# Kernel tuning notes

Hardware: AMD Instinct MI355X
Metric: run time of the kernel (lower is better)

The kernel has to match this reference:

```python
import jax, jax.numpy as jnp
import numpy as np
from jax import lax

EPS = 0.01  # BatchNorm eps from the module

def binarize(x):
    # BinarizeF: >= 0 -> +1, < 0 -> -1
    return jnp.where(x >= 0, 1.0, -1.0).astype(x.dtype)

def bintanh(x):
    # binarize(hardtanh(x)); clip doesn't change sign so forward == sign
    return binarize(jnp.clip(x, -1.0, 1.0))

def bn_nch(x, g, b, m, v):
    # BatchNorm1d eval mode over channel axis of [B, C, L]
    scale = g / jnp.sqrt(v + EPS)
    return (x - m[None, :, None]) * scale[None, :, None] + b[None, :, None]

def bn_nc(x, g, b, m, v):
    scale = g / jnp.sqrt(v + EPS)
    return (x - m[None, :]) * scale[None, :] + b[None, :]

def setup_inputs() -> dict:
    key = jax.random.key(0)
    ks = jax.random.split(key, 32)
    B, CIN, W = 65536, 4, 16
    C, H = 32, 64
    d = {
        'x': jax.random.normal(ks[0], (B, CIN, W), jnp.float32),
        'conv0_w': jax.random.normal(ks[1], (C, CIN, 1), jnp.float32) * 0.1,
        'conv0_b': jax.random.normal(ks[2], (C,), jnp.float32) * 0.01,
        'bn0_g': jax.random.uniform(ks[3], (C,), jnp.float32, 0.5, 1.5),
        'bn0_b': jax.random.normal(ks[4], (C,), jnp.float32) * 0.1,
        'bn0_m': jax.random.normal(ks[5], (C,), jnp.float32) * 0.1,
        'bn0_v': jnp.ones((C,), jnp.float32),
        'convs_w': jax.random.normal(ks[6], (4, C, C, 3), jnp.float32) * 0.1,
        'convs_b': jax.random.normal(ks[7], (4, C), jnp.float32) * 0.01,
        'bns_g': jax.random.uniform(ks[8], (4, C), jnp.float32, 0.5, 1.5),
        'bns_b': jax.random.normal(ks[9], (4, C), jnp.float32) * 0.1,
        'bns_m': jax.random.normal(ks[10], (4, C), jnp.float32) * 0.1,
        'bns_v': jnp.ones((4, C), jnp.float32),
        'fc1_w': jax.random.normal(ks[11], (H, C * W), jnp.float32) * 0.05,
        'fc1_b': jax.random.normal(ks[12], (H,), jnp.float32) * 0.01,
        'bn5_g': jax.random.uniform(ks[13], (H,), jnp.float32, 0.5, 1.5),
        'bn5_b': jax.random.normal(ks[14], (H,), jnp.float32) * 0.1,
        'bn5_m': jax.random.normal(ks[15], (H,), jnp.float32) * 0.1,
        'bn5_v': jnp.ones((H,), jnp.float32),
        'fc2_w': jax.random.normal(ks[16], (H, H), jnp.float32) * 0.1,
        'fc2_b': jax.random.normal(ks[17], (H,), jnp.float32) * 0.01,
        'bn6_g': jax.random.uniform(ks[18], (H,), jnp.float32, 0.5, 1.5),
        'bn6_b': jax.random.normal(ks[19], (H,), jnp.float32) * 0.1,
        'bn6_m': jax.random.normal(ks[20], (H,), jnp.float32) * 0.1,
        'bn6_v': jnp.ones((H,), jnp.float32),
        'fc3_w': jax.random.normal(ks[21], (1, H), jnp.float32) * 0.1,
        'fc3_b': jax.random.normal(ks[22], (1,), jnp.float32) * 0.01,
    }
    return d

def reference(x, conv0_w, conv0_b, bn0_g, bn0_b, bn0_m, bn0_v,
              convs_w, convs_b, bns_g, bns_b, bns_m, bns_v,
              fc1_w, fc1_b, bn5_g, bn5_b, bn5_m, bn5_v,
              fc2_w, fc2_b, bn6_g, bn6_b, bn6_m, bn6_v,
              fc3_w, fc3_b):
    B = x.shape[0]
    x = x.reshape(-1, 4, 16)  # (B, n_inputs, word_size)
    # conv0: kernel_size=1 binarized conv -> pointwise channel mix
    y = jnp.einsum('bci,oc->boi', x, binarize(conv0_w[:, :, 0])) + conv0_b[None, :, None]
    y = bintanh(bn_nch(y, bn0_g, bn0_b, bn0_m, bn0_v))
    shortcut = y
    dn = ('NCH', 'OIH', 'NCH')
    for i in range(convs_w.shape[0]):  # numLayers - 1 = 4 fixed blocks
        z = lax.conv_general_dilated(y, binarize(convs_w[i]), (1,), ((1, 1),),
                                     dimension_numbers=dn)
        z = z + convs_b[i][None, :, None]
        z = bn_nch(z, bns_g[i], bns_b[i], bns_m[i], bns_v[i])
        y = bintanh(z) + shortcut  # residual add to first block output
    f = y.reshape(B, -1)  # (B, 32*16)
    h = bintanh(bn_nc(f @ binarize(fc1_w).T + fc1_b, bn5_g, bn5_b, bn5_m, bn5_v))
    h = bintanh(bn_nc(h @ binarize(fc2_w).T + fc2_b, bn6_g, bn6_b, bn6_m, bn6_v))
    out = jax.nn.sigmoid(h @ binarize(fc3_w).T + fc3_b)  # (B, 1)
    return out
```

## Files before the change

### kernel.cpp

```cpp
#include <hip/hip_runtime.h>
#include <hip/hip_bf16.h>
#include <math.h>

typedef unsigned int uint;

#define WB4   0
#define L1S   512
#define L1T   640
#define W1T   672
#define T5O   1696
#define W2T   1760
#define T6O   1888
#define W3O   1952
#define FB3O  1954
#define TOTW  1955

#define ST5   (T5O - W1T)
#define SW2   (W2T - W1T)
#define ST6   (T6O - W1T)
#define SW3   (W3O - W1T)
#define SFB3  (FB3O - W1T)
#define SMTOT (TOTW - W1T)

__device__ __forceinline__ float bnr(float v, float cb, float m, float sc, float b) {
  return __fadd_rn(__fmul_rn(__fsub_rn(__fadd_rn(v, cb), m), sc), b);
}

__device__ __forceinline__ int ibs(int lo, int hi, int dir,
                                   float cb, float m, float sc, float b) {
  int ans = hi + 1;
  while (lo <= hi) {
    int mid = lo + ((hi - lo) >> 1);
    float vf = (float)(dir ? -mid : mid);
    if (bnr(vf, cb, m, sc, b) >= 0.f) { ans = mid; hi = mid - 1; }
    else lo = mid + 1;
  }
  return ans;
}

__device__ __forceinline__ float key2f(uint k) {
  return __uint_as_float((k & 0x80000000u) ? (k ^ 0x80000000u) : ~k);
}

__device__ __forceinline__ float fsearch(int dir, float cb, float m, float sc, float b) {
  uint lo = 0x00800000u;
  uint hi = 0xFF7FFFFFu;
  float fhi = key2f(hi);
  if (!(bnr(dir ? -fhi : fhi, cb, m, sc, b) >= 0.f))
    return __uint_as_float(0x7F800000u);
  while (lo < hi) {
    uint mid = lo + ((hi - lo) >> 1);
    float fm = key2f(mid);
    if (bnr(dir ? -fm : fm, cb, m, sc, b) >= 0.f) hi = mid; else lo = mid + 1;
  }
  return key2f(lo);
}

__global__ void prep_kernel(
    const float* __restrict__ conv0_w, const float* __restrict__ conv0_b,
    const float* __restrict__ bn0_g, const float* __restrict__ bn0_b,
    const float* __restrict__ bn0_m, const float* __restrict__ bn0_v,
    const float* __restrict__ convs_w, const float* __restrict__ convs_b,
    const float* __restrict__ bns_g, const float* __restrict__ bns_b,
    const float* __restrict__ bns_m, const float* __restrict__ bns_v,
    const float* __restrict__ fc1_w, const float* __restrict__ fc1_b,
    const float* __restrict__ bn5_g, const float* __restrict__ bn5_b,
    const float* __restrict__ bn5_m, const float* __restrict__ bn5_v,
    const float* __restrict__ fc2_w, const float* __restrict__ fc2_b,
    const float* __restrict__ bn6_g, const float* __restrict__ bn6_b,
    const float* __restrict__ bn6_m, const float* __restrict__ bn6_v,
    const float* __restrict__ fc3_w, const float* __restrict__ fc3_b,
    uint* __restrict__ ws)
{
  const int t0 = blockIdx.x * blockDim.x + threadIdx.x;
  const int NT = gridDim.x * blockDim.x;
  for (int task = t0; task < 1443; task += NT) {
    if (task < 32) {
      int o = task;
      float sc = bn0_g[o] / sqrtf(bn0_v[o] + 0.01f);
      int dir = sc < 0.f;
      uint fm = dir ? 0x80000000u : 0u;
      uint4 sg;
      sg.x = ((conv0_w[o*4+0] >= 0.f) ? 0u : 0x80000000u) ^ fm;
      sg.y = ((conv0_w[o*4+1] >= 0.f) ? 0u : 0x80000000u) ^ fm;
      sg.z = ((conv0_w[o*4+2] >= 0.f) ? 0u : 0x80000000u) ^ fm;
      sg.w = ((conv0_w[o*4+3] >= 0.f) ? 0u : 0x80000000u) ^ fm;
      ((uint4*)(ws + L1S))[o] = sg;
      ((float*)(ws + L1T))[o] = fsearch(dir, conv0_b[o], bn0_m[o], sc, bn0_b[o]);
    } else if (task < 160) {
      int idx = task - 32, k = idx >> 5, o = idx & 31, ko = k * 32 + o;
      float sc = bns_g[ko] / sqrtf(bns_v[ko] + 0.01f);
      int dir = sc < 0.f;
      uint fm = dir ? 0xFFFFFFFFu : 0u;
      uint wv[3];
      for (int d = 0; d < 3; ++d) {
        uint w = 0;
        for (int c = 0; c < 32; ++c)
          if (convs_w[(ko * 32 + c) * 3 + d] >= 0.f) w |= 1u << c;
        wv[d] = w ^ fm;
      }
      int T = ibs(-384, 384, dir, convs_b[ko], bns_m[ko], sc, bns_b[ko]);
      uint4 pk; pk.x = wv[0]; pk.y = wv[1]; pk.z = wv[2]; pk.w = (uint)T;
      ((uint4*)(ws + WB4))[ko] = pk;
    } else if (task < 1184) {
      int u = task - 160, i = u >> 6, j = u & 63;
      float sc = bn5_g[j] / sqrtf(bn5_v[j] + 0.01f);
      uint fm = (sc < 0.f) ? 0xFFFFFFFFu : 0u;
      uint w = 0;
      for (int c = 0; c < 32; ++c)
        if (fc1_w[j * 512 + c * 16 + i] >= 0.f) w |= 1u << c;
      int slot = j * 16 + ((((i >> 2) ^ ((j >> 3) & 3)) << 2) | (i & 3));
      ws[W1T + slot] = w ^ fm;
    } else if (task < 1248) {
      int j = task - 1184;
      float sc = bn5_g[j] / sqrtf(bn5_v[j] + 0.01f);
      int dir = sc < 0.f;
      ((int*)ws)[T5O + j] = ibs(-1025, 1025, dir, fc1_b[j], bn5_m[j], sc, bn5_b[j]);
    } else if (task < 1376) {
      int u = task - 1248, h = u >> 6, j = u & 63;
      float sc = bn6_g[j] / sqrtf(bn6_v[j] + 0.01f);
      uint fm = (sc < 0.f) ? 0xFFFFFFFFu : 0u;
      uint w = 0;
      for (int c = 0; c < 32; ++c)
        if (fc2_w[j * 64 + h * 32 + c] >= 0.f) w |= 1u << c;
      ws[W2T + h * 64 + j] = w ^ fm;
    } else if (task < 1440) {
      int j = task - 1376;
      float sc = bn6_g[j] / sqrtf(bn6_v[j] + 0.01f);
      int dir = sc < 0.f;
      ((int*)ws)[T6O + j] = ibs(-65, 65, dir, fc2_b[j], bn6_m[j], sc, bn6_b[j]);
    } else if (task < 1442) {
      int h = task - 1440;
      uint w = 0;
      for (int c = 0; c < 32; ++c)
        if (fc3_w[h * 32 + c] >= 0.f) w |= 1u << c;
      ws[W3O + h] = w;
    } else {
      ((float*)ws)[FB3O] = fc3_b[0];
    }
  }
}

__global__ __launch_bounds__(256, 6) void bnn_kernel(const float* __restrict__ x,
                                                     const uint* __restrict__ ws,
                                                     float* __restrict__ out,
                                                     int B)
{
  __shared__ uint sm[SMTOT];
  for (int i = threadIdx.x; i < SMTOT; i += 256) sm[i] = ws[W1T + i];
  __syncthreads();
  const int gt = blockIdx.x * 256 + threadIdx.x;
  const int b = gt >> 3;
  const int l = gt & 7;
  if (b >= B) return;
  const bool hasL = (l > 0), hasR = (l < 7);
  const uint mL = hasL ? ~0u : 0u;
  const uint mR = hasR ? ~0u : 0u;

  uint xu0[4], xu1[4];
  const float2* xp = (const float2*)(x + (size_t)b * 64 + 2 * l);
#pragma unroll
  for (int c = 0; c < 4; ++c) {
    float2 v = xp[c * 8];
    xu0[c] = __float_as_uint(v.x);
    xu1[c] = __float_as_uint(v.y);
  }

  const uint4* l1s = (const uint4*)(ws + L1S);
  const float* l1t = (const float*)(ws + L1T);
  uint s0v0 = 0, s0v1 = 0;
  for (int o = 31; o >= 0; --o) {
    uint4 sg = l1s[o];
    float tf = l1t[o];
    float d0 = __fadd_rn(__fadd_rn(__fadd_rn(
                  __uint_as_float(xu0[0] ^ sg.x),
                  __uint_as_float(xu0[1] ^ sg.y)),
                  __uint_as_float(xu0[2] ^ sg.z)),
                  __uint_as_float(xu0[3] ^ sg.w));
    float d1 = __fadd_rn(__fadd_rn(__fadd_rn(
                  __uint_as_float(xu1[0] ^ sg.x),
                  __uint_as_float(xu1[1] ^ sg.y)),
                  __uint_as_float(xu1[2] ^ sg.z)),
                  __uint_as_float(xu1[3] ^ sg.w));
    s0v0 = s0v0 + s0v0 + (uint)(d0 >= tf);
    s0v1 = s0v1 + s0v1 + (uint)(d1 >= tf);
  }

  const uint s0l = (uint)__shfl_up((int)s0v1, 1);
  const uint s0r = (uint)__shfl_down((int)s0v0, 1);

  uint cur0, cur1;

  {
    const int M0 = hasL ? 96 : 64;
    const int M1 = hasR ? 96 : 64;
    const uint4* wb4 = (const uint4*)(ws + WB4);
    uint n0 = 0, n1 = 0;
    for (int o = 31; o >= 0; --o) {
      uint4 w = wb4[o];
      int T = (int)w.w;
      int pc0 = __popc(s0v0 ^ w.y) + __popc((s0l ^ w.x) & mL) + __popc(s0v1 ^ w.z);
      int pc1 = __popc(s0v1 ^ w.y) + __popc(s0v0 ^ w.x) + __popc((s0r ^ w.z) & mR);
      n0 = n0 + n0 + (uint)(M0 - 2 * pc0 >= T);
      n1 = n1 + n1 + (uint)(M1 - 2 * pc1 >= T);
    }
    cur0 = n0; cur1 = n1;
  }

  for (int k = 1; k < 4; ++k) {
    const uint cl = (uint)__shfl_up((int)cur1, 1);
    const uint cr = (uint)__shfl_down((int)cur0, 1);
    const uint e0 = ~(cur0 ^ s0v0);
    const uint e1 = ~(cur1 ^ s0v1);
    const uint el = (~(cl ^ s0l)) & mL;
    const uint er = (~(cr ^ s0r)) & mR;
    const int pe0 = __popc(e0), pe1 = __popc(e1);
    const int P2_0 = 2 * (__popc(el) + pe0 + pe1);
    const int P2_1 = 2 * (pe0 + pe1 + __popc(er));
    const uint4* wb4 = (const uint4*)(ws + WB4) + k * 32;
    uint n0 = 0, n1 = 0;
    for (int o = 31; o >= 0; --o) {
      uint4 w = wb4[o];
      int T = (int)w.w;
      int pc0 = __popc((cur0 ^ w.y) & e0) + __popc((cl ^ w.x) & el)
              + __popc((cur1 ^ w.z) & e1);
      int pc1 = __popc((cur1 ^ w.y) & e1) + __popc((cur0 ^ w.x) & e0)
              + __popc((cr ^ w.z) & er);
      n0 = n0 + n0 + (uint)(P2_0 - 4 * pc0 >= T);
      n1 = n1 + n1 + (uint)(P2_1 - 4 * pc1 >= T);
    }
    cur0 = n0; cur1 = n1;
  }

  const int gbase = (threadIdx.x & 63) & ~7;
  uint curF[16], eF[16];
  int E = 0;
#pragma unroll
  for (int i = 0; i < 16; ++i) {
    int src = gbase + (i >> 1);
    uint cw = (uint)__shfl((i & 1) ? (int)cur1 : (int)cur0, src);
    uint sw = (uint)__shfl((i & 1) ? (int)s0v1 : (int)s0v0, src);
    curF[i] = cw;
    eF[i] = ~(cw ^ sw);
    E += __popc(eF[i]);
  }
  const int E2 = 2 * E;

  const uint4* smq = (const uint4*)sm;
  const int swz = l & 3;
  uint hbits = 0;
  for (int jj = 7; jj >= 0; --jj) {
    int j = l * 8 + jj;
    int pc = 0;
#pragma unroll
    for (int c = 0; c < 4; ++c) {
      uint4 w4 = smq[j * 4 + (c ^ swz)];
      pc += __popc((curF[c*4+0] ^ w4.x) & eF[c*4+0]);
      pc += __popc((curF[c*4+1] ^ w4.y) & eF[c*4+1]);
      pc += __popc((curF[c*4+2] ^ w4.z) & eF[c*4+2]);
      pc += __popc((curF[c*4+3] ^ w4.w) & eF[c*4+3]);
    }
    hbits = hbits + hbits + (uint)(E2 - 4 * pc >= (int)sm[ST5 + j]);
  }
  uint hh = hbits << ((l & 3) * 8);
  uint h0 = (l < 4) ? hh : 0u;
  uint h1 = (l < 4) ? 0u : hh;
  h0 |= (uint)__shfl_xor((int)h0, 1); h0 |= (uint)__shfl_xor((int)h0, 2); h0 |= (uint)__shfl_xor((int)h0, 4);
  h1 |= (uint)__shfl_xor((int)h1, 1); h1 |= (uint)__shfl_xor((int)h1, 2); h1 |= (uint)__shfl_xor((int)h1, 4);

  uint gbits = 0;
  for (int jj = 7; jj >= 0; --jj) {
    int j = l * 8 + jj;
    int pc = __popc(h0 ^ sm[SW2 + j]) + __popc(h1 ^ sm[SW2 + 64 + j]);
    gbits = gbits + gbits + (uint)(64 - 2 * pc >= (int)sm[ST6 + j]);
  }
  uint gg = gbits << ((l & 3) * 8);
  uint g0 = (l < 4) ? gg : 0u;
  uint g1 = (l < 4) ? 0u : gg;
  g0 |= (uint)__shfl_xor((int)g0, 1); g0 |= (uint)__shfl_xor((int)g0, 2); g0 |= (uint)__shfl_xor((int)g0, 4);
  g1 |= (uint)__shfl_xor((int)g1, 1); g1 |= (uint)__shfl_xor((int)g1, 2); g1 |= (uint)__shfl_xor((int)g1, 4);

  if (l == 0) {
    int pc = __popc(g0 ^ sm[SW3]) + __popc(g1 ^ sm[SW3 + 1]);
    float z = __fadd_rn((float)(64 - 2 * pc), __uint_as_float(sm[SFB3]));
    out[b] = 1.f / (1.f + expf(-z));
  }
}

extern "C" void kernel_launch(void* const* d_in, const int* in_sizes, int n_in,
                              void* d_out, int out_size, void* d_ws, size_t ws_size,
                              hipStream_t stream) {
  const float* x       = (const float*)d_in[0];
  const float* conv0_w = (const float*)d_in[1];
  const float* conv0_b = (const float*)d_in[2];
  const float* bn0_g   = (const float*)d_in[3];
  const float* bn0_b   = (const float*)d_in[4];
  const float* bn0_m   = (const float*)d_in[5];
  const float* bn0_v   = (const float*)d_in[6];
  const float* convs_w = (const float*)d_in[7];
  const float* convs_b = (const float*)d_in[8];
  const float* bns_g   = (const float*)d_in[9];
  const float* bns_b   = (const float*)d_in[10];
  const float* bns_m   = (const float*)d_in[11];
  const float* bns_v   = (const float*)d_in[12];
  const float* fc1_w   = (const float*)d_in[13];
  const float* fc1_b   = (const float*)d_in[14];
  const float* bn5_g   = (const float*)d_in[15];
  const float* bn5_b   = (const float*)d_in[16];
  const float* bn5_m   = (const float*)d_in[17];
  const float* bn5_v   = (const float*)d_in[18];
  const float* fc2_w   = (const float*)d_in[19];
  const float* fc2_b   = (const float*)d_in[20];
  const float* bn6_g   = (const float*)d_in[21];
  const float* bn6_b   = (const float*)d_in[22];
  const float* bn6_m   = (const float*)d_in[23];
  const float* bn6_v   = (const float*)d_in[24];
  const float* fc3_w   = (const float*)d_in[25];
  const float* fc3_b   = (const float*)d_in[26];
  uint* ws = (uint*)d_ws;

  hipLaunchKernelGGL(prep_kernel, dim3(6), dim3(256), 0, stream,
                     conv0_w, conv0_b, bn0_g, bn0_b, bn0_m, bn0_v,
                     convs_w, convs_b, bns_g, bns_b, bns_m, bns_v,
                     fc1_w, fc1_b, bn5_g, bn5_b, bn5_m, bn5_v,
                     fc2_w, fc2_b, bn6_g, bn6_b, bn6_m, bn6_v,
                     fc3_w, fc3_b, ws);

  const int B = in_sizes[0] / 64;
  const int threads = B * 8;
  hipLaunchKernelGGL(bnn_kernel, dim3((threads + 255) / 256), dim3(256), 0, stream,
                     x, ws, (float*)d_out, B);
}
```

Baseline: 182.0 us.

## Stage all packed weights in LDS, prefetch x early, use ds_swizzle gathers

All packed weight tables, including the conv0 sign and conv-block tables, are now copied into shared memory, where before those were read from global memory. The x loads are issued before the LDS fill and barrier so their latency overlaps the copy. The 16-way shuffle gather becomes ds_swizzle broadcasts, and the loops are fully unrolled with precomputed LDS pointers. Occupancy hint rises to 8 blocks per CU, at the cost of more shared memory per block and possible register pressure from unrolling.

New measurement: 180.0 us. No clear change (-1.1%).

```diff
diff --git a/kernel.cpp b/kernel.cpp
--- a/kernel.cpp
+++ b/kernel.cpp
@@ -14,13 +14,6 @@
 #define W3O   1952
 #define FB3O  1954
 #define TOTW  1955
-
-#define ST5   (T5O - W1T)
-#define SW2   (W2T - W1T)
-#define ST6   (T6O - W1T)
-#define SW3   (W3O - W1T)
-#define SFB3  (FB3O - W1T)
-#define SMTOT (TOTW - W1T)
 
 __device__ __forceinline__ float bnr(float v, float cb, float m, float sc, float b) {
   return __fadd_rn(__fmul_rn(__fsub_rn(__fadd_rn(v, cb), m), sc), b);
@@ -141,34 +134,41 @@
   }
 }
 
-__global__ __launch_bounds__(256, 6) void bnn_kernel(const float* __restrict__ x,
+#define SWZB(v, g) ((uint)__builtin_amdgcn_ds_swizzle((int)(v), ((g) << 5) | 0x18))
+
+__global__ __launch_bounds__(256, 8) void bnn_kernel(const float* __restrict__ x,
                                                      const uint* __restrict__ ws,
                                                      float* __restrict__ out,
                                                      int B)
 {
-  __shared__ uint sm[SMTOT];
-  for (int i = threadIdx.x; i < SMTOT; i += 256) sm[i] = ws[W1T + i];
-  __syncthreads();
+  __shared__ __align__(16) uint sm[TOTW];
   const int gt = blockIdx.x * 256 + threadIdx.x;
   const int b = gt >> 3;
   const int l = gt & 7;
+
+  uint xu0[4], xu1[4];
+  if (b < B) {
+    const float2* xp = (const float2*)(x + (size_t)b * 64 + 2 * l);
+#pragma unroll
+    for (int c = 0; c < 4; ++c) {
+      float2 v = xp[c * 8];
+      xu0[c] = __float_as_uint(v.x);
+      xu1[c] = __float_as_uint(v.y);
+    }
+  }
+
+  for (int i = threadIdx.x; i < TOTW; i += 256) sm[i] = ws[i];
+  __syncthreads();
   if (b >= B) return;
+
   const bool hasL = (l > 0), hasR = (l < 7);
   const uint mL = hasL ? ~0u : 0u;
   const uint mR = hasR ? ~0u : 0u;
 
-  uint xu0[4], xu1[4];
-  const float2* xp = (const float2*)(x + (size_t)b * 64 + 2 * l);
-#pragma unroll
-  for (int c = 0; c < 4; ++c) {
-    float2 v = xp[c * 8];
-    xu0[c] = __float_as_uint(v.x);
-    xu1[c] = __float_as_uint(v.y);
-  }
-
-  const uint4* l1s = (const uint4*)(ws + L1S);
-  const float* l1t = (const float*)(ws + L1T);
+  const uint4* l1s = (const uint4*)(sm + L1S);
+  const float* l1t = (const float*)(sm + L1T);
   uint s0v0 = 0, s0v1 = 0;
+#pragma unroll
   for (int o = 31; o >= 0; --o) {
     uint4 sg = l1s[o];
     float tf = l1t[o];
@@ -194,8 +194,9 @@
   {
     const int M0 = hasL ? 96 : 64;
     const int M1 = hasR ? 96 : 64;
-    const uint4* wb4 = (const uint4*)(ws + WB4);
+    const uint4* wb4 = (const uint4*)(sm + WB4);
     uint n0 = 0, n1 = 0;
+#pragma unroll
     for (int o = 31; o >= 0; --o) {
       uint4 w = wb4[o];
       int T = (int)w.w;
@@ -217,8 +218,9 @@
     const int pe0 = __popc(e0), pe1 = __popc(e1);
     const int P2_0 = 2 * (__popc(el) + pe0 + pe1);
     const int P2_1 = 2 * (pe0 + pe1 + __popc(er));
-    const uint4* wb4 = (const uint4*)(ws + WB4) + k * 32;
+    const uint4* wb4 = (const uint4*)(sm + WB4) + k * 32;
     uint n0 = 0, n1 = 0;
+#pragma unroll
     for (int o = 31; o >= 0; --o) {
       uint4 w = wb4[o];
       int T = (int)w.w;
@@ -232,35 +234,49 @@
     cur0 = n0; cur1 = n1;
   }
 
-  const int gbase = (threadIdx.x & 63) & ~7;
   uint curF[16], eF[16];
   int E = 0;
-#pragma unroll
-  for (int i = 0; i < 16; ++i) {
-    int src = gbase + (i >> 1);
-    uint cw = (uint)__shfl((i & 1) ? (int)cur1 : (int)cur0, src);
-    uint sw = (uint)__shfl((i & 1) ? (int)s0v1 : (int)s0v0, src);
-    curF[i] = cw;
-    eF[i] = ~(cw ^ sw);
-    E += __popc(eF[i]);
-  }
+#define GAT(g) { \
+    uint cw0 = SWZB(cur0, g), cw1 = SWZB(cur1, g); \
+    uint sw0 = SWZB(s0v0, g), sw1 = SWZB(s0v1, g); \
+    curF[2*(g)]   = cw0; eF[2*(g)]   = ~(cw0 ^ sw0); \
+    curF[2*(g)+1] = cw1; eF[2*(g)+1] = ~(cw1 ^ sw1); \
+    E += __popc(eF[2*(g)]) + __popc(eF[2*(g)+1]); }
+  GAT(0) GAT(1) GAT(2) GAT(3) GAT(4) GAT(5) GAT(6) GAT(7)
+#undef GAT
   const int E2 = 2 * E;
 
-  const uint4* smq = (const uint4*)sm;
   const int swz = l & 3;
+  const uint4* pA = (const uint4*)(sm + W1T + l * 128 + ((0 ^ swz) << 2));
+  const uint4* pB = (const uint4*)(sm + W1T + l * 128 + ((1 ^ swz) << 2));
+  const uint4* pC = (const uint4*)(sm + W1T + l * 128 + ((2 ^ swz) << 2));
+  const uint4* pD = (const uint4*)(sm + W1T + l * 128 + ((3 ^ swz) << 2));
+  const int jb = l * 8;
   uint hbits = 0;
+#pragma unroll
   for (int jj = 7; jj >= 0; --jj) {
-    int j = l * 8 + jj;
+    uint4 wA = pA[jj * 4];
+    uint4 wB = pB[jj * 4];
+    uint4 wC = pC[jj * 4];
+    uint4 wD = pD[jj * 4];
     int pc = 0;
-#pragma unroll
-    for (int c = 0; c < 4; ++c) {
-      uint4 w4 = smq[j * 4 + (c ^ swz)];
-      pc += __popc((curF[c*4+0] ^ w4.x) & eF[c*4+0]);
-      pc += __popc((curF[c*4+1] ^ w4.y) & eF[c*4+1]);
-      pc += __popc((curF[c*4+2] ^ w4.z) & eF[c*4+2]);
-      pc += __popc((curF[c*4+3] ^ w4.w) & eF[c*4+3]);
-    }
-    hbits = hbits + hbits + (uint)(E2 - 4 * pc >= (int)sm[ST5 + j]);
+    pc += __popc((curF[0]  ^ wA.x) & eF[0]);
+    pc += __popc((curF[1]  ^ wA.y) & eF[1]);
+    pc += __popc((curF[2]  ^ wA.z) & eF[2]);
+    pc += __popc((curF[3]  ^ wA.w) & eF[3]);
+    pc += __popc((curF[4]  ^ wB.x) & eF[4]);
+    pc += __popc((curF[5]  ^ wB.y) & eF[5]);
+    pc += __popc((curF[6]  ^ wB.z) & eF[6]);
+    pc += __popc((curF[7]  ^ wB.w) & eF[7]);
+    pc += __popc((curF[8]  ^ wC.x) & eF[8]);
+    pc += __popc((curF[9]  ^ wC.y) & eF[9]);
+    pc += __popc((curF[10] ^ wC.z) & eF[10]);
+    pc += __popc((curF[11] ^ wC.w) & eF[11]);
+    pc += __popc((curF[12] ^ wD.x) & eF[12]);
+    pc += __popc((curF[13] ^ wD.y) & eF[13]);
+    pc += __popc((curF[14] ^ wD.z) & eF[14]);
+    pc += __popc((curF[15] ^ wD.w) & eF[15]);
+    hbits = hbits + hbits + (uint)(E2 - 4 * pc >= (int)sm[T5O + jb + jj]);
   }
   uint hh = hbits << ((l & 3) * 8);
   uint h0 = (l < 4) ? hh : 0u;
@@ -269,10 +285,10 @@
   h1 |= (uint)__shfl_xor((int)h1, 1); h1 |= (uint)__shfl_xor((int)h1, 2); h1 |= (uint)__shfl_xor((int)h1, 4);
 
   uint gbits = 0;
+#pragma unroll
   for (int jj = 7; jj >= 0; --jj) {
-    int j = l * 8 + jj;
-    int pc = __popc(h0 ^ sm[SW2 + j]) + __popc(h1 ^ sm[SW2 + 64 + j]);
-    gbits = gbits + gbits + (uint)(64 - 2 * pc >= (int)sm[ST6 + j]);
+    int pc = __popc(h0 ^ sm[W2T + jb + jj]) + __popc(h1 ^ sm[W2T + 64 + jb + jj]);
+    gbits = gbits + gbits + (uint)(64 - 2 * pc >= (int)sm[T6O + jb + jj]);
   }
   uint gg = gbits << ((l & 3) * 8);
   uint g0 = (l < 4) ? gg : 0u;
@@ -281,8 +297,8 @@
   g1 |= (uint)__shfl_xor((int)g1, 1); g1 |= (uint)__shfl_xor((int)g1, 2); g1 |= (uint)__shfl_xor((int)g1, 4);
 
   if (l == 0) {
-    int pc = __popc(g0 ^ sm[SW3]) + __popc(g1 ^ sm[SW3 + 1]);
-    float z = __fadd_rn((float)(64 - 2 * pc), __uint_as_float(sm[SFB3]));
+    int pc = __popc(g0 ^ sm[W3O]) + __popc(g1 ^ sm[W3O + 1]);
+    float z = __fadd_rn((float)(64 - 2 * pc), __uint_as_float(sm[FB3O]));
     out[b] = 1.f / (1.f + expf(-z));
   }
 }
```
